# Kernel optimization log

Hardware: AMD Instinct MI355X
Metric: run time of the kernel (lower is better)

Reference implementation:

```python
import jax, jax.numpy as jnp
import numpy as np

L = 6      # layers (enc and dec)
D = 512    # d_model
H = 8      # heads
DK = D // H
F = 2048   # dim_feedforward
B = 8
S = 512    # src len
T = 512    # tgt len
NEG = -1e9


def setup_inputs() -> dict:
    key = jax.random.key(0)
    ks = jax.random.split(key, 64)
    it = iter(ks)
    def w(shape, scale=0.02):
        return jax.random.normal(next(it), shape, dtype=jnp.float32) * scale
    inp = {}
    inp['src'] = jax.random.normal(next(it), (B, S, D), dtype=jnp.float32)
    inp['tgt'] = jax.random.normal(next(it), (B, T, D), dtype=jnp.float32)
    inp['tgt_mask'] = jnp.where(jnp.triu(jnp.ones((T, T), bool), 1), jnp.float32(NEG), jnp.float32(0.0))
    # encoder params (stacked over L layers)
    inp['enc_Wq'] = w((L, H, D, DK)); inp['enc_Wk'] = w((L, H, D, DK)); inp['enc_Wv'] = w((L, H, D, DK))
    inp['enc_Wo'] = w((L, D, D))
    inp['enc_ln1_a'] = jnp.ones((L, D)); inp['enc_ln1_b'] = jnp.zeros((L, D))
    inp['enc_W1'] = w((L, D, F)); inp['enc_b1'] = jnp.zeros((L, F))
    inp['enc_W2'] = w((L, F, D)); inp['enc_b2'] = jnp.zeros((L, D))
    inp['enc_ln2_a'] = jnp.ones((L, D)); inp['enc_ln2_b'] = jnp.zeros((L, D))
    # decoder params
    inp['dec_sWq'] = w((L, H, D, DK)); inp['dec_sWk'] = w((L, H, D, DK)); inp['dec_sWv'] = w((L, H, D, DK))
    inp['dec_sWo'] = w((L, D, D))
    inp['dec_ln1_a'] = jnp.ones((L, D)); inp['dec_ln1_b'] = jnp.zeros((L, D))
    inp['dec_cWq'] = w((L, H, D, DK)); inp['dec_cWk'] = w((L, H, D, DK)); inp['dec_cWv'] = w((L, H, D, DK))
    inp['dec_cWo'] = w((L, D, D))
    inp['dec_ln2_a'] = jnp.ones((L, D)); inp['dec_ln2_b'] = jnp.zeros((L, D))
    inp['dec_W1'] = w((L, D, F)); inp['dec_b1'] = jnp.zeros((L, F))
    inp['dec_W2'] = w((L, F, D)); inp['dec_b2'] = jnp.zeros((L, D))
    inp['dec_ln3_a'] = jnp.ones((L, D)); inp['dec_ln3_b'] = jnp.zeros((L, D))
    return inp


def layernorm(x, a, b):
    # faithful to the torch module: unbiased std (ddof=1) and eps added to std
    mean = x.mean(-1, keepdims=True)
    std = jnp.std(x, axis=-1, keepdims=True, ddof=1)
    return a * (x - mean) / (std + 1e-6) + b


def mha(qx, kx, vx, Wq, Wk, Wv, Wo, mask):
    # Wq/Wk/Wv: [H, D, dk] (per-head torch loop fused into one batched einsum)
    q = jnp.einsum('bsd,hdk->bhsk', qx, Wq)
    k = jnp.einsum('bsd,hdk->bhsk', kx, Wk)
    v = jnp.einsum('bsd,hdk->bhsk', vx, Wv)
    scores = jnp.einsum('bhqk,bhmk->bhqm', q, k) / np.float32(np.sqrt(Wq.shape[-1]))
    if mask is not None:
        scores = scores + mask  # [T,T] broadcasts over batch and heads
    attn = jax.nn.softmax(scores, axis=-1)
    o = jnp.einsum('bhqm,bhmk->bhqk', attn, v)
    b_, h_, s_, k_ = o.shape
    o = o.transpose(0, 2, 1, 3).reshape(b_, s_, h_ * k_)  # concat heads
    return o @ Wo


def ffn(x, W1, b1, W2, b2):
    return jnp.maximum(x @ W1 + b1, 0.0) @ W2 + b2


def reference(src, tgt, tgt_mask,
              enc_Wq, enc_Wk, enc_Wv, enc_Wo, enc_ln1_a, enc_ln1_b,
              enc_W1, enc_b1, enc_W2, enc_b2, enc_ln2_a, enc_ln2_b,
              dec_sWq, dec_sWk, dec_sWv, dec_sWo, dec_ln1_a, dec_ln1_b,
              dec_cWq, dec_cWk, dec_cWv, dec_cWo, dec_ln2_a, dec_ln2_b,
              dec_W1, dec_b1, dec_W2, dec_b2, dec_ln3_a, dec_ln3_b):
    # encoder
    x = src
    for i in range(L):
        h = x + mha(x, x, x, enc_Wq[i], enc_Wk[i], enc_Wv[i], enc_Wo[i], None)
        x = layernorm(h, enc_ln1_a[i], enc_ln1_b[i])
        h = x + ffn(x, enc_W1[i], enc_b1[i], enc_W2[i], enc_b2[i])
        x = layernorm(h, enc_ln2_a[i], enc_ln2_b[i])
    memory = x
    # decoder
    y = tgt
    for i in range(L):
        h = y + mha(y, y, y, dec_sWq[i], dec_sWk[i], dec_sWv[i], dec_sWo[i], tgt_mask)
        y = layernorm(h, dec_ln1_a[i], dec_ln1_b[i])
        h = y + mha(y, memory, memory, dec_cWq[i], dec_cWk[i], dec_cWv[i], dec_cWo[i], None)
        y = layernorm(h, dec_ln2_a[i], dec_ln2_b[i])
        h = y + ffn(y, dec_W1[i], dec_b1[i], dec_W2[i], dec_b2[i])
        y = layernorm(h, dec_ln3_a[i], dec_ln3_b[i])
    return y
```

## Files before the change

### kernel.cpp

```cpp
#include <hip/hip_runtime.h>
#include <hip/hip_bf16.h>

typedef unsigned short u16;
typedef __hip_bfloat16 hbf;
typedef __bf16 bf16x8 __attribute__((ext_vector_type(8)));
typedef float f32x4 __attribute__((ext_vector_type(4)));

#define LL 6
#define DD 512
#define HH 8
#define DKK 64
#define FF 2048
#define BB 8
#define SS 512

#define GLL(gp, lp)                                                        \
  __builtin_amdgcn_global_load_lds(                                        \
      (const __attribute__((address_space(1))) void*)(gp),                 \
      (__attribute__((address_space(3))) void*)(lp), 16, 0, 0)

__global__ __launch_bounds__(256) void cvt_k(const float* __restrict__ x,
                                             hbf* __restrict__ y, int n) {
  for (int i = (blockIdx.x * 256 + threadIdx.x) * 4; i < n; i += gridDim.x * 1024) {
    float4 v = *(const float4*)(x + i);
    y[i] = __float2bfloat16(v.x);
    y[i + 1] = __float2bfloat16(v.y);
    y[i + 2] = __float2bfloat16(v.z);
    y[i + 3] = __float2bfloat16(v.w);
  }
}

__global__ __launch_bounds__(256) void transpose_k(const float* __restrict__ src,
                                                   hbf* __restrict__ dst, int R, int C) {
  __shared__ hbf tile[64][65];
  const int b = blockIdx.z;
  src += (size_t)b * R * C;
  dst += (size_t)b * R * C;
  int c0 = blockIdx.x * 64, r0 = blockIdx.y * 64;
  int tx = threadIdx.x & 63;
  int ty = threadIdx.x >> 6;
#pragma unroll
  for (int i = 0; i < 16; i++) {
    int r = ty + i * 4;
    tile[r][tx] = __float2bfloat16(src[(size_t)(r0 + r) * C + c0 + tx]);
  }
  __syncthreads();
#pragma unroll
  for (int i = 0; i < 16; i++) {
    int r = ty + i * 4;
    dst[(size_t)(c0 + r) * R + r0 + tx] = tile[tx][r];
  }
}

__global__ __launch_bounds__(256) void transpose_qkv_k(const float* __restrict__ Wq,
                                                       const float* __restrict__ Wk,
                                                       const float* __restrict__ Wv,
                                                       hbf* __restrict__ dst) {
  __shared__ hbf tile[64][65];
  const int z = blockIdx.z;
  const int l = z / 24, r = z - l * 24;
  const int zw = r >> 3, h = r & 7;
  const float* src =
      (zw == 0 ? Wq : (zw == 1 ? Wk : Wv)) + ((size_t)l * HH + h) * DD * DKK;
  const int r0 = blockIdx.y * 64;
  const int tx = threadIdx.x & 63, ty = threadIdx.x >> 6;
#pragma unroll
  for (int i = 0; i < 16; i++) {
    int rr = ty + i * 4;
    tile[rr][tx] = __float2bfloat16(src[(size_t)(r0 + rr) * DKK + tx]);
  }
  __syncthreads();
  hbf* d = dst + (size_t)l * 3 * DD * DD + ((size_t)zw * 512 + h * 64) * DD + r0;
#pragma unroll
  for (int i = 0; i < 16; i++) {
    int rr = ty + i * 4;
    d[(size_t)rr * DD + tx] = tile[tx][rr];
  }
}

template <int MODE, int SPLITK>
__global__ __launch_bounds__(256) void gemm_nt(
    const u16* __restrict__ A, const u16* __restrict__ Bm, void* __restrict__ Cout,
    void* __restrict__ C2, void* __restrict__ C3,
    const float* __restrict__ bias, const hbf* __restrict__ res,
    int M, int N, int K, int lda, int ldb, int ldc, int ncoloff,
    long sAo, long sAi, long sBo, long sBi, long sCo, long sCi, int inner, float scale) {
  constexpr int BM = 64, BN = 64, BK = 128;
  __shared__ u16 As[BM * BK];
  __shared__ u16 Bs[BN * BK];

  int g = blockIdx.z;
  int ks = 0;
  if (SPLITK > 1) {
    ks = g;
    g = 0;
  }
  int outer = g / inner, inr = g - outer * inner;
  A += outer * sAo + inr * sAi;
  Bm += outer * sBo + inr * sBi;

  const int tid = threadIdx.x;
  const int m0 = blockIdx.y * BM, n0 = (blockIdx.x + ncoloff) * BN;
  const int wave = tid >> 6, lane = tid & 63;
  const int wm = (wave >> 1) * 32, wn = (wave & 1) * 32;
  const int m16 = lane & 15, quad = lane >> 4;
  const int ld4 = lane >> 4, ln16 = lane & 15;

  const u16* Ab = A + (size_t)m0 * lda;
  const u16* Bb = Bm + (size_t)n0 * ldb;

  f32x4 acc[2][2] = {};

  const int kbeg = ks * (K / SPLITK), kend = kbeg + K / SPLITK;
  for (int k0 = kbeg; k0 < kend; k0 += BK) {
#pragma unroll
    for (int c = 0; c < 4; c++) {
      const int chunk = wave * 4 + c;
      const int row = chunk * 4 + ld4;
      const int scol = (ln16 ^ (((c & 1) << 2) | ld4)) << 3;
      GLL(Ab + (size_t)row * lda + k0 + scol, &As[chunk * 512]);
      GLL(Bb + (size_t)row * ldb + k0 + scol, &Bs[chunk * 512]);
    }
    __syncthreads();
#pragma unroll
    for (int kc = 0; kc < 4; kc++) {
      bf16x8 af[2], bfv[2];
      const int sw = (((kc << 2) | quad) ^ (m16 & 7)) << 3;
#pragma unroll
      for (int i = 0; i < 2; i++)
        af[i] = *(const bf16x8*)(&As[(wm + i * 16 + m16) * 128 + sw]);
#pragma unroll
      for (int j = 0; j < 2; j++)
        bfv[j] = *(const bf16x8*)(&Bs[(wn + j * 16 + m16) * 128 + sw]);
#pragma unroll
      for (int i = 0; i < 2; i++)
#pragma unroll
        for (int j = 0; j < 2; j++)
          acc[i][j] = __builtin_amdgcn_mfma_f32_16x16x32_bf16(af[i], bfv[j], acc[i][j], 0, 0, 0);
    }
    __syncthreads();
  }

#pragma unroll
  for (int i = 0; i < 2; i++) {
#pragma unroll
    for (int j = 0; j < 2; j++) {
      const int col = n0 + wn + j * 16 + m16;
      const int rowb = m0 + wm + i * 16 + quad * 4;
#pragma unroll
      for (int r = 0; r < 4; r++) {
        const int row = rowb + r;
        float v = acc[i][j][r] * scale;
        if (MODE == 0) {
          hbf* C = (hbf*)Cout + outer * sCo + inr * sCi;
          C[(size_t)row * ldc + col] = __float2bfloat16(v);
        } else if (MODE == 2) {
          float* C = (float*)((SPLITK > 1 && ks == 1) ? C2 : Cout);
          C += outer * sCo + inr * sCi;
          if (SPLITK == 1 || ks == 0) {
            if (bias) v += bias[col];
            if (res) v += __bfloat162float(res[(size_t)row * ldc + col]);
          }
          C[(size_t)row * ldc + col] = v;
        } else if (MODE == 3) {
          hbf* C = (hbf*)Cout + outer * sCo + inr * sCi;
          v += bias[col];
          C[(size_t)row * ldc + col] = __float2bfloat16(fmaxf(v, 0.0f));
        } else if (MODE == 4) {
          const int b = row >> 9, s = row & 511;
          const int which = col >> 9, h = (col >> 6) & 7, dk = col & 63;
          const int bh = (b << 3) + h;
          if (which == 0)
            ((hbf*)Cout)[((size_t)bh * SS + s) * DKK + dk] = __float2bfloat16(v * 0.125f);
          else if (which == 1)
            ((hbf*)C2)[((size_t)bh * SS + s) * DKK + dk] = __float2bfloat16(v);
          else
            ((hbf*)C3)[((size_t)bh * DKK + dk) * SS + s] = __float2bfloat16(v);
        }
      }
    }
  }
}

__global__ __launch_bounds__(256) void flash_k(const u16* __restrict__ Q,
                                               const u16* __restrict__ Kb,
                                               const u16* __restrict__ Vt,
                                               hbf* __restrict__ O, int causal) {
  __shared__ u16 Qs[32][72];
  __shared__ u16 Ks[128 * 72];
  __shared__ u16 Ss[32][520];
  const int bh = blockIdx.y;
  const int q0 = blockIdx.x * 32;
  const int b = bh >> 3, h = bh & 7;
  const int tid = threadIdx.x;
  const int wave = tid >> 6, lane = tid & 63;
  const int m16 = lane & 15, quad = lane >> 4;
  const int rg = (wave >> 1) * 16;
  const int chf = wave & 1;

  const u16* Qp = Q + ((size_t)bh * SS + q0) * DKK;
  const u16* Kp = Kb + (size_t)bh * SS * DKK;
  const u16* Vp = Vt + (size_t)bh * DKK * SS;

  {
    int row = tid >> 3, ch = (tid & 7) << 3;
    *(float4*)(&Qs[row][ch]) = *(const float4*)(Qp + (size_t)row * DKK + ch);
  }

  for (int kt = 0; kt < 4; kt++) {
    if (kt > 0) __syncthreads();
#pragma unroll
    for (int p = 0; p < 4; p++) {
      int idx = p * 256 + tid;
      int row = idx >> 3, ch = (idx & 7) << 3;
      *(float4*)(&Ks[row * 72 + ch]) =
          *(const float4*)(Kp + (size_t)(kt * 128 + row) * DKK + ch);
    }
    __syncthreads();
#pragma unroll
    for (int ct = 0; ct < 4; ct++) {
      f32x4 s{};
#pragma unroll
      for (int kc = 0; kc < 2; kc++) {
        bf16x8 a = *(const bf16x8*)(&Qs[rg + m16][kc * 32 + quad * 8]);
        bf16x8 bv =
            *(const bf16x8*)(&Ks[(chf * 64 + ct * 16 + m16) * 72 + kc * 32 + quad * 8]);
        s = __builtin_amdgcn_mfma_f32_16x16x32_bf16(a, bv, s, 0, 0, 0);
      }
      const int colb = kt * 128 + chf * 64 + ct * 16 + m16;
#pragma unroll
      for (int r = 0; r < 4; r++)
        *((hbf*)&Ss[rg + quad * 4 + r][colb]) = __float2bfloat16(s[r]);
    }
  }
  __syncthreads();

#pragma unroll
  for (int rr = 0; rr < 8; rr++) {
    const int r = wave * 8 + rr;
    const int gr = q0 + r;
    float v[8];
#pragma unroll
    for (int i = 0; i < 8; i++) {
      const int col = lane + i * 64;
      v[i] = __bfloat162float(((const hbf*)Ss[r])[col]);
      if (causal && col > gr) v[i] = -1e30f;
    }
    float m = v[0];
#pragma unroll
    for (int i = 1; i < 8; i++) m = fmaxf(m, v[i]);
#pragma unroll
    for (int off = 1; off < 64; off <<= 1) m = fmaxf(m, __shfl_xor(m, off));
    float e[8], s = 0.f;
#pragma unroll
    for (int i = 0; i < 8; i++) {
      e[i] = __expf(v[i] - m);
      s += e[i];
    }
#pragma unroll
    for (int off = 1; off < 64; off <<= 1) s += __shfl_xor(s, off);
    const float inv = 1.0f / s;
#pragma unroll
    for (int i = 0; i < 8; i++)
      ((hbf*)Ss[r])[lane + i * 64] = __float2bfloat16(e[i] * inv);
  }
  __syncthreads();

  f32x4 o[2] = {};
  u16* Vs = Ks;
  for (int vt = 0; vt < 4; vt++) {
    if (vt > 0) __syncthreads();
#pragma unroll
    for (int p = 0; p < 4; p++) {
      int idx = p * 256 + tid;
      int row = idx >> 4, ch = (idx & 15) << 3;
      *(float4*)(&Vs[row * 136 + ch]) =
          *(const float4*)(Vp + (size_t)row * SS + vt * 128 + ch);
    }
    __syncthreads();
#pragma unroll
    for (int kc = 0; kc < 4; kc++) {
      bf16x8 a = *(const bf16x8*)(&Ss[rg + m16][vt * 128 + kc * 32 + quad * 8]);
#pragma unroll
      for (int dt = 0; dt < 2; dt++) {
        bf16x8 bv =
            *(const bf16x8*)(&Vs[(chf * 32 + dt * 16 + m16) * 136 + kc * 32 + quad * 8]);
        o[dt] = __builtin_amdgcn_mfma_f32_16x16x32_bf16(a, bv, o[dt], 0, 0, 0);
      }
    }
  }
#pragma unroll
  for (int dt = 0; dt < 2; dt++) {
    const int d = h * 64 + chf * 32 + dt * 16 + m16;
#pragma unroll
    for (int r = 0; r < 4; r++) {
      const int row = q0 + rg + quad * 4 + r;
      O[(size_t)b * SS * DD + (size_t)row * DD + d] = __float2bfloat16(o[dt][r]);
    }
  }
}

template <typename T>
__global__ __launch_bounds__(256) void layernorm_k(const float* __restrict__ X,
                                                   const float* __restrict__ X2,
                                                   const float* __restrict__ ga,
                                                   const float* __restrict__ gb,
                                                   T* __restrict__ out, int Dn) {
  const int row = blockIdx.x;
  X += (size_t)row * Dn;
  X2 += (size_t)row * Dn;
  out += (size_t)row * Dn;
  const int t = threadIdx.x;
  float2 xv = *(const float2*)(X + 2 * t);
  float2 x2 = *(const float2*)(X2 + 2 * t);
  xv.x += x2.x;
  xv.y += x2.y;
  float s = xv.x + xv.y, ss = xv.x * xv.x + xv.y * xv.y;
#pragma unroll
  for (int off = 32; off > 0; off >>= 1) {
    s += __shfl_down(s, off);
    ss += __shfl_down(ss, off);
  }
  __shared__ float sm[8];
  __shared__ float smean, sinv;
  const int wv = t >> 6, ln = t & 63;
  if (ln == 0) {
    sm[wv] = s;
    sm[4 + wv] = ss;
  }
  __syncthreads();
  if (t == 0) {
    float S1 = sm[0] + sm[1] + sm[2] + sm[3];
    float S2 = sm[4] + sm[5] + sm[6] + sm[7];
    float mean = S1 / Dn;
    float var = (S2 - S1 * mean) / (Dn - 1);
    var = fmaxf(var, 0.0f);
    smean = mean;
    sinv = 1.0f / (sqrtf(var) + 1e-6f);
  }
  __syncthreads();
  const float mean = smean, inv = sinv;
  float o0 = ga[2 * t] * (xv.x - mean) * inv + gb[2 * t];
  float o1 = ga[2 * t + 1] * (xv.y - mean) * inv + gb[2 * t + 1];
  if constexpr (sizeof(T) == 2) {
    out[2 * t] = (T)__float2bfloat16(o0);
    out[2 * t + 1] = (T)__float2bfloat16(o1);
  } else {
    out[2 * t] = o0;
    out[2 * t + 1] = o1;
  }
}

extern "C" void kernel_launch(void* const* d_in, const int* in_sizes, int n_in,
                              void* d_out, int out_size, void* d_ws, size_t ws_size,
                              hipStream_t stream) {
  (void)in_sizes; (void)n_in; (void)out_size;
  const float* src = (const float*)d_in[0];
  const float* tgt = (const float*)d_in[1];
  const float* eWq = (const float*)d_in[3];
  const float* eWk = (const float*)d_in[4];
  const float* eWv = (const float*)d_in[5];
  const float* eWo = (const float*)d_in[6];
  const float* eln1a = (const float*)d_in[7];
  const float* eln1b = (const float*)d_in[8];
  const float* eW1 = (const float*)d_in[9];
  const float* eb1 = (const float*)d_in[10];
  const float* eW2 = (const float*)d_in[11];
  const float* eb2 = (const float*)d_in[12];
  const float* eln2a = (const float*)d_in[13];
  const float* eln2b = (const float*)d_in[14];
  const float* sWq = (const float*)d_in[15];
  const float* sWk = (const float*)d_in[16];
  const float* sWv = (const float*)d_in[17];
  const float* sWo = (const float*)d_in[18];
  const float* dln1a = (const float*)d_in[19];
  const float* dln1b = (const float*)d_in[20];
  const float* cWq = (const float*)d_in[21];
  const float* cWk = (const float*)d_in[22];
  const float* cWv = (const float*)d_in[23];
  const float* cWo = (const float*)d_in[24];
  const float* dln2a = (const float*)d_in[25];
  const float* dln2b = (const float*)d_in[26];
  const float* dW1 = (const float*)d_in[27];
  const float* db1 = (const float*)d_in[28];
  const float* dW2 = (const float*)d_in[29];
  const float* db2 = (const float*)d_in[30];
  const float* dln3a = (const float*)d_in[31];
  const float* dln3b = (const float*)d_in[32];

  const size_t MB = 1024 * 1024;
  char* ws = (char*)d_ws;
  const size_t QKV_L = (size_t)3 * DD * DD;
  const size_t WO_L = (size_t)DD * DD;
  const size_t WF_L = (size_t)DD * FF;
  const bool preT = ws_size >= 150 * MB;

  hbf *qkvT_all = nullptr, *woT_all = nullptr, *w1T_all = nullptr, *w2T_all = nullptr;
  hbf *wqkvS = nullptr, *woS = nullptr, *w1S = nullptr, *w2S = nullptr;
  char* actb;
  if (preT) {
    qkvT_all = (hbf*)(ws);
    woT_all = (hbf*)(ws + 28311552);
    w1T_all = (hbf*)(ws + 37748736);
    w2T_all = (hbf*)(ws + 62914560);
    actb = ws + 84 * MB;
  } else {
    if (ws_size < 72 * MB) return;
    wqkvS = (hbf*)(ws);
    woS = (hbf*)(ws + 2 * MB);
    w1S = (hbf*)(ws + 2 * MB + 512 * 1024);
    w2S = (hbf*)(ws + 4 * MB + 512 * 1024);
    actb = ws + 7 * MB;
  }
  hbf* sbuf = (hbf*)(actb);
  u16* xbuf = (u16*)(actb + 4 * MB);
  hbf* tbuf = (hbf*)(actb + 8 * MB);
  u16* ybuf = (u16*)(actb + 12 * MB);
  u16* qbuf = (u16*)(actb + 16 * MB);
  u16* kbuf = (u16*)(actb + 20 * MB);
  u16* vtb = (u16*)(actb + 24 * MB);
  u16* obuf = (u16*)(actb + 28 * MB);
  u16* ffnh = (u16*)(actb + 32 * MB);
  float* projf = (float*)(actb + 48 * MB);
  float* projf2 = (float*)(actb + 56 * MB);

  const size_t WQL = (size_t)HH * DD * DKK;
  const size_t WOL = (size_t)DD * DD;
  const size_t WFL = (size_t)DD * FF;

  if (preT) {
    transpose_qkv_k<<<dim3(1, 8, LL * 24), dim3(256), 0, stream>>>(eWq, eWk, eWv, qkvT_all);
    transpose_qkv_k<<<dim3(1, 8, LL * 24), dim3(256), 0, stream>>>(sWq, sWk, sWv,
                                                                   qkvT_all + LL * QKV_L);
    transpose_qkv_k<<<dim3(1, 8, LL * 24), dim3(256), 0, stream>>>(
        cWq, cWk, cWv, qkvT_all + 2 * LL * QKV_L);
    transpose_k<<<dim3(8, 8, LL), dim3(256), 0, stream>>>(eWo, woT_all, DD, DD);
    transpose_k<<<dim3(8, 8, LL), dim3(256), 0, stream>>>(sWo, woT_all + LL * WO_L, DD, DD);
    transpose_k<<<dim3(8, 8, LL), dim3(256), 0, stream>>>(cWo, woT_all + 2 * LL * WO_L, DD, DD);
    transpose_k<<<dim3(32, 8, LL), dim3(256), 0, stream>>>(eW1, w1T_all, DD, FF);
    transpose_k<<<dim3(32, 8, LL), dim3(256), 0, stream>>>(dW1, w1T_all + LL * WF_L, DD, FF);
    transpose_k<<<dim3(8, 32, LL), dim3(256), 0, stream>>>(eW2, w2T_all, FF, DD);
    transpose_k<<<dim3(8, 32, LL), dim3(256), 0, stream>>>(dW2, w2T_all + LL * WF_L, FF, DD);
  }

  auto attention = [&](const u16* qin, const u16* kvin, const hbf* qkvTl, const hbf* woTl,
                       const u16* resid, int causal) {
    if (qin == kvin) {
      gemm_nt<4, 1><<<dim3(24, 64, 1), dim3(256), 0, stream>>>(
          qin, (const u16*)qkvTl, qbuf, kbuf, vtb, nullptr, nullptr, BB * SS, 3 * DD, DD,
          DD, DD, 0, 0, 0, 0, 0, 0, 0, 0, 1, 1.f);
    } else {
      gemm_nt<4, 1><<<dim3(8, 64, 1), dim3(256), 0, stream>>>(
          qin, (const u16*)qkvTl, qbuf, kbuf, vtb, nullptr, nullptr, BB * SS, DD, DD,
          DD, DD, 0, 0, 0, 0, 0, 0, 0, 0, 1, 1.f);
      gemm_nt<4, 1><<<dim3(16, 64, 1), dim3(256), 0, stream>>>(
          kvin, (const u16*)qkvTl, qbuf, kbuf, vtb, nullptr, nullptr, BB * SS, 3 * DD, DD,
          DD, DD, 0, 8, 0, 0, 0, 0, 0, 0, 1, 1.f);
    }
    flash_k<<<dim3(16, 64), dim3(256), 0, stream>>>(qbuf, kbuf, vtb, (hbf*)obuf, causal);
    gemm_nt<2, 2><<<dim3(8, 64, 2), dim3(256), 0, stream>>>(
        obuf, (const u16*)woTl, projf, projf2, nullptr, nullptr, (const hbf*)resid,
        BB * SS, DD, DD, DD, DD, DD, 0, 0, 0, 0, 0, 0, 0, 1, 1.f);
  };

  auto ffn = [&](const u16* xin, const hbf* w1Tl, const float* b1l, const hbf* w2Tl,
                 const float* b2l) {
    gemm_nt<3, 1><<<dim3(32, 64, 1), dim3(256), 0, stream>>>(
        xin, (const u16*)w1Tl, ffnh, nullptr, nullptr, b1l, nullptr, BB * SS, FF, DD,
        DD, DD, FF, 0, 0, 0, 0, 0, 0, 0, 1, 1.f);
    gemm_nt<2, 2><<<dim3(8, 64, 2), dim3(256), 0, stream>>>(
        ffnh, (const u16*)w2Tl, projf, projf2, nullptr, b2l, (const hbf*)xin, BB * SS, DD,
        FF, FF, FF, DD, 0, 0, 0, 0, 0, 0, 0, 1, 1.f);
  };

  auto lnb = [&](const float* X, const float* a, const float* b, u16* out) {
    layernorm_k<hbf><<<dim3(BB * SS), dim3(256), 0, stream>>>(X, projf2, a, b, (hbf*)out, DD);
  };

  cvt_k<<<dim3(2048), dim3(256), 0, stream>>>(src, sbuf, BB * SS * DD);
  cvt_k<<<dim3(2048), dim3(256), 0, stream>>>(tgt, tbuf, BB * SS * DD);

  const u16* cur = (const u16*)sbuf;
  for (int l = 0; l < LL; l++) {
    const hbf *qkvTl, *woTl, *w1Tl, *w2Tl;
    if (preT) {
      qkvTl = qkvT_all + (size_t)l * QKV_L;
      woTl = woT_all + (size_t)l * WO_L;
      w1Tl = w1T_all + (size_t)l * WF_L;
      w2Tl = w2T_all + (size_t)l * WF_L;
    } else {
      transpose_qkv_k<<<dim3(1, 8, 24), dim3(256), 0, stream>>>(
          eWq + l * WQL, eWk + l * WQL, eWv + l * WQL, wqkvS);
      transpose_k<<<dim3(8, 8, 1), dim3(256), 0, stream>>>(eWo + l * WOL, woS, DD, DD);
      qkvTl = wqkvS;
      woTl = woS;
    }
    attention(cur, cur, qkvTl, woTl, cur, 0);
    lnb(projf, eln1a + l * DD, eln1b + l * DD, xbuf);
    if (!preT) {
      transpose_k<<<dim3(32, 8, 1), dim3(256), 0, stream>>>(eW1 + l * WFL, w1S, DD, FF);
      transpose_k<<<dim3(8, 32, 1), dim3(256), 0, stream>>>(eW2 + l * WFL, w2S, FF, DD);
      w1Tl = w1S;
      w2Tl = w2S;
    }
    ffn(xbuf, w1Tl, eb1 + l * FF, w2Tl, eb2 + l * DD);
    lnb(projf, eln2a + l * DD, eln2b + l * DD, xbuf);
    cur = xbuf;
  }
  const u16* mem = cur;
  const u16* yc = (const u16*)tbuf;
  for (int l = 0; l < LL; l++) {
    const hbf *sqkvTl, *swoTl, *cqkvTl, *cwoTl, *w1Tl, *w2Tl;
    if (preT) {
      sqkvTl = qkvT_all + ((size_t)LL + l) * QKV_L;
      swoTl = woT_all + ((size_t)LL + l) * WO_L;
      cqkvTl = qkvT_all + ((size_t)2 * LL + l) * QKV_L;
      cwoTl = woT_all + ((size_t)2 * LL + l) * WO_L;
      w1Tl = w1T_all + ((size_t)LL + l) * WF_L;
      w2Tl = w2T_all + ((size_t)LL + l) * WF_L;
    }
    if (!preT) {
      transpose_qkv_k<<<dim3(1, 8, 24), dim3(256), 0, stream>>>(
          sWq + l * WQL, sWk + l * WQL, sWv + l * WQL, wqkvS);
      transpose_k<<<dim3(8, 8, 1), dim3(256), 0, stream>>>(sWo + l * WOL, woS, DD, DD);
      sqkvTl = wqkvS;
      swoTl = woS;
    }
    attention(yc, yc, sqkvTl, swoTl, yc, 1);
    lnb(projf, dln1a + l * DD, dln1b + l * DD, ybuf);
    yc = ybuf;
    if (!preT) {
      transpose_qkv_k<<<dim3(1, 8, 24), dim3(256), 0, stream>>>(
          cWq + l * WQL, cWk + l * WQL, cWv + l * WQL, wqkvS);
      transpose_k<<<dim3(8, 8, 1), dim3(256), 0, stream>>>(cWo + l * WOL, woS, DD, DD);
      cqkvTl = wqkvS;
      cwoTl = woS;
    }
    attention(yc, mem, cqkvTl, cwoTl, yc, 0);
    lnb(projf, dln2a + l * DD, dln2b + l * DD, ybuf);
    if (!preT) {
      transpose_k<<<dim3(32, 8, 1), dim3(256), 0, stream>>>(dW1 + l * WFL, w1S, DD, FF);
      transpose_k<<<dim3(8, 32, 1), dim3(256), 0, stream>>>(dW2 + l * WFL, w2S, FF, DD);
      w1Tl = w1S;
      w2Tl = w2S;
    }
    ffn(ybuf, w1Tl, db1 + l * FF, w2Tl, db2 + l * DD);
    if (l == LL - 1) {
      layernorm_k<float><<<dim3(BB * SS), dim3(256), 0, stream>>>(
          projf, projf2, dln3a + l * DD, dln3b + l * DD, (float*)d_out, DD);
    } else {
      lnb(projf, dln3a + l * DD, dln3b + l * DD, ybuf);
      yc = ybuf;
    }
  }
}
```

Measured before the change: 2.151 ms.

## Retile GEMM to 2-wave blocks with BM template, BK=64, and XCD-aware block swizzle

The bf16 GEMM kernel is retemplated on BM (64 or 128) and now runs with 128 threads (2 waves). Each wave computes a 32/64-row by 64-column slab, so the B fragments loaded from LDS are reused across more MFMAs, and the K tile shrinks from 128 to 64. A block-index remap spreads consecutive blocks across 8 groups so that tiles sharing operands land on the same XCD/L2. Larger BM is used for the QKV and FFN1 GEMMs to halve the grid. The cost is fewer waves per block, which can reduce latency hiding, and the K loop has twice as many barrier-separated iterations.

```diff
diff --git a/kernel.cpp b/kernel.cpp
--- a/kernel.cpp
+++ b/kernel.cpp
@@ -78,16 +78,29 @@
   }
 }
 
-template <int MODE, int SPLITK>
-__global__ __launch_bounds__(256) void gemm_nt(
+template <int BM, int MODE, int SPLITK>
+__global__ __launch_bounds__(128) void gemm_nt(
     const u16* __restrict__ A, const u16* __restrict__ Bm, void* __restrict__ Cout,
     void* __restrict__ C2, void* __restrict__ C3,
     const float* __restrict__ bias, const hbf* __restrict__ res,
     int M, int N, int K, int lda, int ldb, int ldc, int ncoloff,
     long sAo, long sAi, long sBo, long sBi, long sCo, long sCi, int inner, float scale) {
-  constexpr int BM = 64, BN = 64, BK = 128;
+  constexpr int BN = 64, BK = 64;
+  constexpr int AM = BM / 32;
+  constexpr int NCA = BM / 16;
+  constexpr int WR = BM / 2;
   __shared__ u16 As[BM * BK];
   __shared__ u16 Bs[BN * BK];
+
+  int bxx = blockIdx.x, byy = blockIdx.y;
+  {
+    const int gx = gridDim.x, gy = gridDim.y;
+    const int f = byy * gx + bxx;
+    const int st = gy >> 3;
+    const int rem = f >> 3;
+    byy = (f & 7) * st + rem % st;
+    bxx = rem / st;
+  }
 
   int g = blockIdx.z;
   int ks = 0;
@@ -100,53 +113,57 @@
   Bm += outer * sBo + inr * sBi;
 
   const int tid = threadIdx.x;
-  const int m0 = blockIdx.y * BM, n0 = (blockIdx.x + ncoloff) * BN;
+  const int m0 = byy * BM, n0 = (bxx + ncoloff) * BN;
   const int wave = tid >> 6, lane = tid & 63;
-  const int wm = (wave >> 1) * 32, wn = (wave & 1) * 32;
   const int m16 = lane & 15, quad = lane >> 4;
-  const int ld4 = lane >> 4, ln16 = lane & 15;
+  const int l8 = lane & 7, ld8 = lane >> 3;
+  const int scol = (l8 ^ ld8) << 3;
 
   const u16* Ab = A + (size_t)m0 * lda;
   const u16* Bb = Bm + (size_t)n0 * ldb;
 
-  f32x4 acc[2][2] = {};
+  f32x4 acc[AM][4] = {};
 
   const int kbeg = ks * (K / SPLITK), kend = kbeg + K / SPLITK;
   for (int k0 = kbeg; k0 < kend; k0 += BK) {
 #pragma unroll
+    for (int c = 0; c < NCA; c++) {
+      const int ch = wave * NCA + c;
+      const int row = ch * 8 + ld8;
+      GLL(Ab + (size_t)row * lda + k0 + scol, &As[ch * 512]);
+    }
+#pragma unroll
     for (int c = 0; c < 4; c++) {
-      const int chunk = wave * 4 + c;
-      const int row = chunk * 4 + ld4;
-      const int scol = (ln16 ^ (((c & 1) << 2) | ld4)) << 3;
-      GLL(Ab + (size_t)row * lda + k0 + scol, &As[chunk * 512]);
-      GLL(Bb + (size_t)row * ldb + k0 + scol, &Bs[chunk * 512]);
+      const int ch = wave * 4 + c;
+      const int row = ch * 8 + ld8;
+      GLL(Bb + (size_t)row * ldb + k0 + scol, &Bs[ch * 512]);
     }
     __syncthreads();
 #pragma unroll
-    for (int kc = 0; kc < 4; kc++) {
-      bf16x8 af[2], bfv[2];
+    for (int kc = 0; kc < 2; kc++) {
+      bf16x8 af[AM], bfv[4];
       const int sw = (((kc << 2) | quad) ^ (m16 & 7)) << 3;
 #pragma unroll
-      for (int i = 0; i < 2; i++)
-        af[i] = *(const bf16x8*)(&As[(wm + i * 16 + m16) * 128 + sw]);
-#pragma unroll
-      for (int j = 0; j < 2; j++)
-        bfv[j] = *(const bf16x8*)(&Bs[(wn + j * 16 + m16) * 128 + sw]);
-#pragma unroll
-      for (int i = 0; i < 2; i++)
-#pragma unroll
-        for (int j = 0; j < 2; j++)
+      for (int i = 0; i < AM; i++)
+        af[i] = *(const bf16x8*)(&As[(wave * WR + i * 16 + m16) * 64 + sw]);
+#pragma unroll
+      for (int j = 0; j < 4; j++)
+        bfv[j] = *(const bf16x8*)(&Bs[(j * 16 + m16) * 64 + sw]);
+#pragma unroll
+      for (int i = 0; i < AM; i++)
+#pragma unroll
+        for (int j = 0; j < 4; j++)
           acc[i][j] = __builtin_amdgcn_mfma_f32_16x16x32_bf16(af[i], bfv[j], acc[i][j], 0, 0, 0);
     }
     __syncthreads();
   }
 
 #pragma unroll
-  for (int i = 0; i < 2; i++) {
-#pragma unroll
-    for (int j = 0; j < 2; j++) {
-      const int col = n0 + wn + j * 16 + m16;
-      const int rowb = m0 + wm + i * 16 + quad * 4;
+  for (int i = 0; i < AM; i++) {
+#pragma unroll
+    for (int j = 0; j < 4; j++) {
+      const int col = n0 + j * 16 + m16;
+      const int rowb = m0 + wave * WR + i * 16 + quad * 4;
 #pragma unroll
       for (int r = 0; r < 4; r++) {
         const int row = rowb + r;
@@ -446,29 +463,29 @@
   auto attention = [&](const u16* qin, const u16* kvin, const hbf* qkvTl, const hbf* woTl,
                        const u16* resid, int causal) {
     if (qin == kvin) {
-      gemm_nt<4, 1><<<dim3(24, 64, 1), dim3(256), 0, stream>>>(
+      gemm_nt<128, 4, 1><<<dim3(24, 32, 1), dim3(128), 0, stream>>>(
           qin, (const u16*)qkvTl, qbuf, kbuf, vtb, nullptr, nullptr, BB * SS, 3 * DD, DD,
           DD, DD, 0, 0, 0, 0, 0, 0, 0, 0, 1, 1.f);
     } else {
-      gemm_nt<4, 1><<<dim3(8, 64, 1), dim3(256), 0, stream>>>(
+      gemm_nt<64, 4, 1><<<dim3(8, 64, 1), dim3(128), 0, stream>>>(
           qin, (const u16*)qkvTl, qbuf, kbuf, vtb, nullptr, nullptr, BB * SS, DD, DD,
           DD, DD, 0, 0, 0, 0, 0, 0, 0, 0, 1, 1.f);
-      gemm_nt<4, 1><<<dim3(16, 64, 1), dim3(256), 0, stream>>>(
+      gemm_nt<64, 4, 1><<<dim3(16, 64, 1), dim3(128), 0, stream>>>(
           kvin, (const u16*)qkvTl, qbuf, kbuf, vtb, nullptr, nullptr, BB * SS, 3 * DD, DD,
           DD, DD, 0, 8, 0, 0, 0, 0, 0, 0, 1, 1.f);
     }
     flash_k<<<dim3(16, 64), dim3(256), 0, stream>>>(qbuf, kbuf, vtb, (hbf*)obuf, causal);
-    gemm_nt<2, 2><<<dim3(8, 64, 2), dim3(256), 0, stream>>>(
+    gemm_nt<64, 2, 2><<<dim3(8, 64, 2), dim3(128), 0, stream>>>(
         obuf, (const u16*)woTl, projf, projf2, nullptr, nullptr, (const hbf*)resid,
         BB * SS, DD, DD, DD, DD, DD, 0, 0, 0, 0, 0, 0, 0, 1, 1.f);
   };
 
   auto ffn = [&](const u16* xin, const hbf* w1Tl, const float* b1l, const hbf* w2Tl,
                  const float* b2l) {
-    gemm_nt<3, 1><<<dim3(32, 64, 1), dim3(256), 0, stream>>>(
+    gemm_nt<128, 3, 1><<<dim3(32, 32, 1), dim3(128), 0, stream>>>(
         xin, (const u16*)w1Tl, ffnh, nullptr, nullptr, b1l, nullptr, BB * SS, FF, DD,
         DD, DD, FF, 0, 0, 0, 0, 0, 0, 0, 1, 1.f);
-    gemm_nt<2, 2><<<dim3(8, 64, 2), dim3(256), 0, stream>>>(
+    gemm_nt<64, 2, 2><<<dim3(8, 64, 2), dim3(128), 0, stream>>>(
         ffnh, (const u16*)w2Tl, projf, projf2, nullptr, b2l, (const hbf*)xin, BB * SS, DD,
         FF, FF, FF, DD, 0, 0, 0, 0, 0, 0, 0, 1, 1.f);
   };
```

After: 2.113 ms. No clear change (-1.7%).
